# Optimization experiments

Hardware: AMD Instinct MI355X
Metric: run time of the kernel (lower is better)

The kernel has to match this reference:

```python
import jax, jax.numpy as jnp
import numpy as np

B, T, D, H = 16, 2048, 512, 512  # batch, seq_len, input_dim, hidden_dim


def setup_inputs() -> dict:
    key = jax.random.key(0)
    k1, k2, k3 = jax.random.split(key, 3)
    x = jax.random.normal(k1, (B, T, D), dtype=jnp.float32)
    # vanilla tanh RnnCell parameters
    W_xh = jax.random.normal(k2, (D, H), dtype=jnp.float32) / np.float32(np.sqrt(D))
    W_hh = jax.random.normal(k3, (H, H), dtype=jnp.float32) / np.float32(np.sqrt(H))
    b = jnp.zeros((H,), dtype=jnp.float32)
    # DFA feedback matrix, 'diagonal' init branch: diag(linspace(0,1,H))
    A = jnp.diag(jnp.linspace(0.0, 1.0, H).astype(jnp.float32))
    return {"x": x, "W_xh": W_xh, "W_hh": W_hh, "b": b, "A": A}


def reference(x, W_xh, W_hh, b, A):
    # Forward of DfaRnn: sequential RNN loop. detach() does not change forward
    # values, so this is a plain tanh RNN scan. A only affects the backward.
    Bb = x.shape[0]
    h0 = jnp.zeros((Bb, W_hh.shape[0]), dtype=x.dtype)

    def step(h, xt):
        h_new = jnp.tanh(xt @ W_xh + h @ W_hh + b)
        return h_new, h_new

    _, hs = jax.lax.scan(step, h0, jnp.swapaxes(x, 0, 1))  # [T,B,H]
    return jnp.swapaxes(hs, 0, 1)  # [B,T,H]
```

## Files before the change

### kernel.cpp

```cpp
#include <hip/hip_runtime.h>
#include <cmath>

#define B_ 16
#define T_ 2048
#define D_ 512
#define H_ 512

__global__ __launch_bounds__(256) void gemm_xw(
    const float* __restrict__ x,
    const float* __restrict__ Wxh,
    const float* __restrict__ bias,
    float* __restrict__ out)
{
    const int tid = threadIdx.x;
    const int n0 = blockIdx.x * 128;
    const int m0 = blockIdx.y * 128;

    __shared__ float As[8][132];
    __shared__ float Bs[8][132];

    const int tx = tid & 15, ty = tid >> 4;
    float acc[8][8] = {};

    const int arow = tid >> 1;
    const int akq  = (tid & 1) * 4;
    const int brow = tid >> 5;
    const int bcol = (tid & 31) * 4;

    for (int k0 = 0; k0 < D_; k0 += 8) {
        float4 a4 = *(const float4*)(x + (size_t)(m0 + arow) * D_ + k0 + akq);
        float4 b4 = *(const float4*)(Wxh + (size_t)(k0 + brow) * H_ + n0 + bcol);
        __syncthreads();
        As[akq + 0][arow] = a4.x;
        As[akq + 1][arow] = a4.y;
        As[akq + 2][arow] = a4.z;
        As[akq + 3][arow] = a4.w;
        *(float4*)(&Bs[brow][bcol]) = b4;
        __syncthreads();
#pragma unroll
        for (int kk = 0; kk < 8; ++kk) {
            float4 a0 = *(const float4*)(&As[kk][ty * 8]);
            float4 a1 = *(const float4*)(&As[kk][ty * 8 + 4]);
            float4 b0 = *(const float4*)(&Bs[kk][tx * 8]);
            float4 b1 = *(const float4*)(&Bs[kk][tx * 8 + 4]);
            float a_[8] = {a0.x, a0.y, a0.z, a0.w, a1.x, a1.y, a1.z, a1.w};
            float b_[8] = {b0.x, b0.y, b0.z, b0.w, b1.x, b1.y, b1.z, b1.w};
#pragma unroll
            for (int i = 0; i < 8; ++i)
#pragma unroll
                for (int j = 0; j < 8; ++j) acc[i][j] += a_[i] * b_[j];
        }
    }

    const float4 bv0 = *(const float4*)(bias + n0 + tx * 8);
    const float4 bv1 = *(const float4*)(bias + n0 + tx * 8 + 4);
    const float bb[8] = {bv0.x, bv0.y, bv0.z, bv0.w, bv1.x, bv1.y, bv1.z, bv1.w};
#pragma unroll
    for (int i = 0; i < 8; ++i) {
        const int m = m0 + ty * 8 + i;
        float4 o0, o1;
        o0.x = acc[i][0] + bb[0]; o0.y = acc[i][1] + bb[1];
        o0.z = acc[i][2] + bb[2]; o0.w = acc[i][3] + bb[3];
        o1.x = acc[i][4] + bb[4]; o1.y = acc[i][5] + bb[5];
        o1.z = acc[i][6] + bb[6]; o1.w = acc[i][7] + bb[7];
        *(float4*)(out + (size_t)m * H_ + n0 + tx * 8)     = o0;
        *(float4*)(out + (size_t)m * H_ + n0 + tx * 8 + 4) = o1;
    }
}

__device__ __forceinline__ void bar_lds() {
    asm volatile("s_waitcnt lgkmcnt(0)\n\ts_barrier" ::: "memory");
}

__global__ __launch_bounds__(512, 2) void rnn_rec(
    const float* __restrict__ Whh,
    float* __restrict__ out,
    unsigned long long* __restrict__ ws)
{
    const int tid = threadIdx.x;
    const int b = blockIdx.x & 15;
    const int s = blockIdx.x >> 4;
    const int j = tid & 63;
    const int p = tid >> 6;
    const int col = (s << 6) + j;

    __shared__ float h_lds[H_];
    __shared__ float part[8 * 64];

    float W_reg[64];
    {
        const float* wbase = Whh + (size_t)(p * 64) * H_ + col;
#pragma unroll
        for (int r = 0; r < 64; ++r) {
            const float* addr = wbase + (size_t)r * H_;
            asm volatile("global_load_dword %0, %1, off"
                         : "=v"(W_reg[r]) : "v"(addr));
        }
        asm volatile("s_waitcnt vmcnt(0)" ::: "memory");
    }

    h_lds[tid] = 0.0f;
    __syncthreads();

    float* outb = out + (size_t)b * T_ * H_;
    unsigned long long* wsb = ws + (size_t)b * 2 * H_;

    float xw0 = 0.0f, xw1 = 0.0f, xw2 = 0.0f;
    if (p == 0) {
        xw0 = outb[(size_t)0 * H_ + col];
        xw1 = outb[(size_t)1 * H_ + col];
        xw2 = outb[(size_t)2 * H_ + col];
    }

    for (int t = 0; t < T_; ++t) {
        float acc = 0.0f;
        const float4* hv = (const float4*)(h_lds + (p << 6));
#pragma unroll
        for (int i = 0; i < 16; ++i) {
            float4 h4 = hv[i];
            acc += h4.x * W_reg[4 * i + 0];
            acc += h4.y * W_reg[4 * i + 1];
            acc += h4.z * W_reg[4 * i + 2];
            acc += h4.w * W_reg[4 * i + 3];
        }
        part[tid] = acc;
        bar_lds();

        const unsigned int tag = (unsigned int)(t + 1);
        const int slot = (t + 1) & 1;
        unsigned long long* wslot = wsb + (size_t)slot * H_;

        if (p == 0) {
            asm volatile("s_waitcnt vmcnt(0)" ::: "memory");
            float ssum = xw0;
#pragma unroll
            for (int q = 0; q < 8; ++q) ssum += part[q * 64 + j];
            union { unsigned int u; float f; } cv;
            cv.f = tanhf(ssum);
            unsigned long long pv =
                ((unsigned long long)tag << 32) | (unsigned long long)cv.u;
            (void)__hip_atomic_exchange(wslot + col, pv, __ATOMIC_RELAXED,
                                        __HIP_MEMORY_SCOPE_AGENT);
            outb[(size_t)t * H_ + col] = cv.f;
            h_lds[col] = cv.f;
            xw0 = xw1;
            xw1 = xw2;
            xw2 = (t + 3 < T_) ? outb[(size_t)(t + 3) * H_ + col] : 0.0f;
        } else {
            const int q = (p == s) ? 0 : p;
            unsigned long long* src = wslot + (q << 6) + j;
            unsigned long long v;
            do {
                v = __hip_atomic_load(src, __ATOMIC_RELAXED,
                                      __HIP_MEMORY_SCOPE_AGENT);
            } while ((unsigned int)(v >> 32) < tag);
            union { unsigned int u; float f; } cv;
            cv.u = (unsigned int)v;
            h_lds[(q << 6) + j] = cv.f;
        }
        bar_lds();
    }
}

extern "C" void kernel_launch(void* const* d_in, const int* in_sizes, int n_in,
                              void* d_out, int out_size, void* d_ws,
                              size_t ws_size, hipStream_t stream) {
    const float* x    = (const float*)d_in[0];
    const float* Wxh  = (const float*)d_in[1];
    const float* Whh  = (const float*)d_in[2];
    const float* bias = (const float*)d_in[3];
    float* out = (float*)d_out;

    hipMemsetAsync(d_ws, 0, (size_t)B_ * 2 * H_ * sizeof(unsigned long long),
                   stream);

    dim3 ggrid(H_ / 128, (B_ * T_) / 128, 1);
    gemm_xw<<<ggrid, 256, 0, stream>>>(x, Wxh, bias, out);

    rnn_rec<<<128, 512, 0, stream>>>(Whh, out, (unsigned long long*)d_ws);
}
```

Measured before the change: 2.989 ms.

## Replace LDS partial-sum reduction with wave shuffles and double-buffer hidden state

Each wave now owns 8 output columns. Its 8 lane groups each take a 64-row slice of the recurrent matvec and reduce across groups with xor shuffles, replacing the LDS partial buffer and one barrier per timestep. The hidden state is double-buffered in LDS so only one barrier per step is needed, and every wave both produces its columns and polls one remote slice. The W row indices are rotated per lane group to avoid LDS bank conflicts. The cost is lower ALU utilisation for the tanh/store (8 lanes per wave) and a more complex indexing scheme.

```diff
diff --git a/kernel.cpp b/kernel.cpp
--- a/kernel.cpp
+++ b/kernel.cpp
@@ -80,84 +80,88 @@
     const int tid = threadIdx.x;
     const int b = blockIdx.x & 15;
     const int s = blockIdx.x >> 4;
-    const int j = tid & 63;
-    const int p = tid >> 6;
-    const int col = (s << 6) + j;
+    const int w = tid >> 6;
+    const int l = tid & 63;
+    const int g = l >> 3;
+    const int cl = l & 7;
+    const int c_glob = (s << 6) + (w << 3) + cl;
+    const int grot = g << 3;
 
-    __shared__ float h_lds[H_];
-    __shared__ float part[8 * 64];
+    __shared__ float h_lds[2][H_];
 
     float W_reg[64];
     {
-        const float* wbase = Whh + (size_t)(p * 64) * H_ + col;
 #pragma unroll
         for (int r = 0; r < 64; ++r) {
-            const float* addr = wbase + (size_t)r * H_;
+            const int row = (g << 6) + ((grot + r) & 63);
+            const float* addr = Whh + (size_t)row * H_ + c_glob;
             asm volatile("global_load_dword %0, %1, off"
                          : "=v"(W_reg[r]) : "v"(addr));
         }
         asm volatile("s_waitcnt vmcnt(0)" ::: "memory");
     }
 
-    h_lds[tid] = 0.0f;
+    h_lds[0][tid] = 0.0f;
     __syncthreads();
 
     float* outb = out + (size_t)b * T_ * H_;
     unsigned long long* wsb = ws + (size_t)b * 2 * H_;
 
+    const int c_pref = (s << 6) + (w << 3) + l;
     float xw0 = 0.0f, xw1 = 0.0f, xw2 = 0.0f;
-    if (p == 0) {
-        xw0 = outb[(size_t)0 * H_ + col];
-        xw1 = outb[(size_t)1 * H_ + col];
-        xw2 = outb[(size_t)2 * H_ + col];
+    if (l < 8) {
+        xw0 = outb[(size_t)0 * H_ + c_pref];
+        xw1 = outb[(size_t)1 * H_ + c_pref];
+        xw2 = outb[(size_t)2 * H_ + c_pref];
     }
 
+    const int q = (w < 7) ? (w + (w >= s ? 1 : 0)) : -1;
+
     for (int t = 0; t < T_; ++t) {
+        const float* hb = h_lds[t & 1];
         float acc = 0.0f;
-        const float4* hv = (const float4*)(h_lds + (p << 6));
 #pragma unroll
         for (int i = 0; i < 16; ++i) {
-            float4 h4 = hv[i];
-            acc += h4.x * W_reg[4 * i + 0];
-            acc += h4.y * W_reg[4 * i + 1];
-            acc += h4.z * W_reg[4 * i + 2];
-            acc += h4.w * W_reg[4 * i + 3];
+            const int idx = (g << 6) + ((grot + (i << 2)) & 63);
+            const float4 h4 = *(const float4*)(hb + idx);
+            acc += h4.x * W_reg[4 * i + 0] + h4.y * W_reg[4 * i + 1]
+                 + h4.z * W_reg[4 * i + 2] + h4.w * W_reg[4 * i + 3];
         }
-        part[tid] = acc;
-        bar_lds();
+        acc += __shfl_xor(acc, 8);
+        acc += __shfl_xor(acc, 16);
+        acc += __shfl_xor(acc, 32);
 
         const unsigned int tag = (unsigned int)(t + 1);
         const int slot = (t + 1) & 1;
         unsigned long long* wslot = wsb + (size_t)slot * H_;
+        float* hn = h_lds[(t + 1) & 1];
 
-        if (p == 0) {
-            asm volatile("s_waitcnt vmcnt(0)" ::: "memory");
-            float ssum = xw0;
-#pragma unroll
-            for (int q = 0; q < 8; ++q) ssum += part[q * 64 + j];
+        if (l < 8) {
             union { unsigned int u; float f; } cv;
-            cv.f = tanhf(ssum);
+            cv.f = tanhf(acc + xw0);
             unsigned long long pv =
                 ((unsigned long long)tag << 32) | (unsigned long long)cv.u;
-            (void)__hip_atomic_exchange(wslot + col, pv, __ATOMIC_RELAXED,
-                                        __HIP_MEMORY_SCOPE_AGENT);
-            outb[(size_t)t * H_ + col] = cv.f;
-            h_lds[col] = cv.f;
+            __hip_atomic_store(wslot + c_pref, pv, __ATOMIC_RELAXED,
+                               __HIP_MEMORY_SCOPE_AGENT);
+            outb[(size_t)t * H_ + c_pref] = cv.f;
+            hn[c_pref] = cv.f;
             xw0 = xw1;
             xw1 = xw2;
-            xw2 = (t + 3 < T_) ? outb[(size_t)(t + 3) * H_ + col] : 0.0f;
-        } else {
-            const int q = (p == s) ? 0 : p;
-            unsigned long long* src = wslot + (q << 6) + j;
+            xw2 = (t + 3 < T_) ? outb[(size_t)(t + 3) * H_ + c_pref] : 0.0f;
+        }
+
+        if (q >= 0) {
+            unsigned long long* src = wslot + (q << 6) + l;
             unsigned long long v;
             do {
                 v = __hip_atomic_load(src, __ATOMIC_RELAXED,
                                       __HIP_MEMORY_SCOPE_AGENT);
             } while ((unsigned int)(v >> 32) < tag);
-            union { unsigned int u; float f; } cv;
-            cv.u = (unsigned int)v;
-            h_lds[(q << 6) + j] = cv.f;
+            union { unsigned int u; float f; } cv2;
+            cv2.u = (unsigned int)v;
+            hn[(q << 6) + l] = cv2.f;
         }
+
         bar_lds();
     }
 }
```

Measured after the change: 2.896 ms. -3.1%, faster.
